# Kernel tuning notes

Measured on AMD Instinct MI355X. Metric: run time of the kernel, lower is better.

The kernel has to match this reference:

```python
import jax, jax.numpy as jnp
import numpy as np

DIM = 2048
DIM_SEQ = 2048
DIM_OUT = DIM // 2
LN_EPS = 1e-5


def setup_inputs() -> dict:
    key = jax.random.key(0)
    k1, k2 = jax.random.split(key)
    x = jax.random.normal(k1, (8, DIM_SEQ, DIM), dtype=jnp.float32)
    init_eps = 0.001 / DIM_SEQ
    # Conv1d(dim_seq, dim_seq, 1) weight -> [seq, seq] seq-mixing matrix
    proj_w = jax.random.uniform(k2, (DIM_SEQ, DIM_SEQ), minval=-init_eps, maxval=init_eps, dtype=jnp.float32)
    proj_b = jnp.ones((DIM_SEQ,), dtype=jnp.float32)
    ln_scale = jnp.ones((DIM_OUT,), dtype=jnp.float32)
    ln_bias = jnp.zeros((DIM_OUT,), dtype=jnp.float32)
    return {"x": x, "proj_w": proj_w, "proj_b": proj_b, "ln_scale": ln_scale, "ln_bias": ln_bias}


def reference(x, proj_w, proj_b, ln_scale, ln_bias):
    # chunk into residual and gate halves along feature dim
    res, gate = jnp.split(x, 2, axis=-1)  # each [b, s, d/2]
    # LayerNorm over last dim of gate
    mu = jnp.mean(gate, axis=-1, keepdims=True)
    var = jnp.mean(jnp.square(gate - mu), axis=-1, keepdims=True)
    gate = (gate - mu) * jax.lax.rsqrt(var + LN_EPS) * ln_scale + ln_bias
    # Conv1d kernel=1 over seq axis == seq-mixing matmul: [s,t] x [b,t,d] -> [b,s,d]
    gate = jnp.einsum('st,btd->bsd', proj_w, gate) + proj_b[None, :, None]
    # act = Identity; gated residual multiply
    return gate * res
```

## Files before the change

### kernel.cpp

```cpp
#include <hip/hip_runtime.h>

typedef __attribute__((ext_vector_type(8))) short short8;
typedef __attribute__((ext_vector_type(4))) float floatx4;

__device__ __forceinline__ unsigned short f2bf(float f) {
    unsigned int u = __builtin_bit_cast(unsigned int, f);
    u += 0x7fffu + ((u >> 16) & 1u);
    return (unsigned short)(u >> 16);
}

__device__ __forceinline__ void async16(unsigned short* lds, const unsigned short* g) {
    __builtin_amdgcn_global_load_lds(
        (__attribute__((address_space(1))) void*)(g),
        (__attribute__((address_space(3))) void*)(lds),
        16, 0, 0);
}

#define DIM      2048
#define DSEQ     2048
#define DOUT     1024
#define NBATCH   8
#define NKB      (DSEQ / 32)

__global__ __launch_bounds__(256) void cast_w_kernel(const float* __restrict__ w,
                                                     unsigned short* __restrict__ o) {
    int i = (blockIdx.x * 256 + threadIdx.x) * 4;
    int s = i >> 11;
    int t = i & 2047;
    float4 v = *(const float4*)(w + i);
    unsigned int lo = (unsigned int)f2bf(v.x) | ((unsigned int)f2bf(v.y) << 16);
    unsigned int hi = (unsigned int)f2bf(v.z) | ((unsigned int)f2bf(v.w) << 16);
    unsigned short* dst = o + (((size_t)(t >> 5)) * DSEQ + s) * 32 + (t & 31);
    *(uint2*)dst = make_uint2(lo, hi);
}

__global__ __launch_bounds__(256) void ln_t_kernel(const float* __restrict__ X,
                                                   const float* __restrict__ lns,
                                                   const float* __restrict__ lnb,
                                                   unsigned short* __restrict__ Gt) {
    const int tid  = threadIdx.x;
    const int wave = tid >> 6;
    const int lane = tid & 63;
    const int t0   = blockIdx.x * 32;
    const int b    = blockIdx.y;

    __shared__ unsigned short lt[32][1028];

    #pragma unroll
    for (int i = 0; i < 8; ++i) {
        const int r = wave * 8 + i;
        const float* xr = X + ((size_t)(b * DSEQ + t0 + r)) * DIM + DOUT;
        float4 v[4];
        float s = 0.f, ss = 0.f;
        #pragma unroll
        for (int c = 0; c < 4; ++c) {
            v[c] = *(const float4*)(xr + c * 256 + lane * 4);
            s  += v[c].x + v[c].y + v[c].z + v[c].w;
            ss += v[c].x * v[c].x + v[c].y * v[c].y + v[c].z * v[c].z + v[c].w * v[c].w;
        }
        #pragma unroll
        for (int off = 32; off > 0; off >>= 1) {
            s  += __shfl_xor(s,  off, 64);
            ss += __shfl_xor(ss, off, 64);
        }
        const float mu  = s * (1.f / 1024.f);
        const float var = ss * (1.f / 1024.f) - mu * mu;
        const float inv = rsqrtf(var + 1e-5f);
        #pragma unroll
        for (int c = 0; c < 4; ++c) {
            const int d = c * 256 + lane * 4;
            float4 sc = *(const float4*)(lns + d);
            float4 bi = *(const float4*)(lnb + d);
            float y0 = (v[c].x - mu) * inv * sc.x + bi.x;
            float y1 = (v[c].y - mu) * inv * sc.y + bi.y;
            float y2 = (v[c].z - mu) * inv * sc.z + bi.z;
            float y3 = (v[c].w - mu) * inv * sc.w + bi.w;
            unsigned int lo = (unsigned int)f2bf(y0) | ((unsigned int)f2bf(y1) << 16);
            unsigned int hi = (unsigned int)f2bf(y2) | ((unsigned int)f2bf(y3) << 16);
            *(uint2*)&lt[r][d] = make_uint2(lo, hi);
        }
    }
    __syncthreads();

    #pragma unroll
    for (int it = 0; it < 4; ++it) {
        const int d = it * 256 + tid;
        unsigned int u[16];
        #pragma unroll
        for (int j = 0; j < 16; ++j)
            u[j] = (unsigned int)lt[2 * j][d] | ((unsigned int)lt[2 * j + 1][d] << 16);
        uint4* dst = (uint4*)(Gt + (((size_t)b * NKB + (t0 >> 5)) * DOUT + d) * 32);
        dst[0] = make_uint4(u[0],  u[1],  u[2],  u[3]);
        dst[1] = make_uint4(u[4],  u[5],  u[6],  u[7]);
        dst[2] = make_uint4(u[8],  u[9],  u[10], u[11]);
        dst[3] = make_uint4(u[12], u[13], u[14], u[15]);
    }
}

#define BM 128
#define BN 128
#define BK 64

__global__ __launch_bounds__(256) void gemm_sgu(const unsigned short* __restrict__ Wt,
                                                const unsigned short* __restrict__ Gt,
                                                const float* __restrict__ X,
                                                const float* __restrict__ Pb,
                                                float* __restrict__ Out) {
    const int tid = threadIdx.x;
    const int s0  = blockIdx.x * BM;
    const int d0  = blockIdx.y * BN;
    const int b   = blockIdx.z;

    __shared__ unsigned short As[2 * BM * 32];
    __shared__ unsigned short Bs[2 * BN * 32];

    const int wave = tid >> 6;
    const int lane = tid & 63;
    const int wr   = wave >> 1;
    const int wc   = wave & 1;
    const int ln15 = lane & 15;
    const int q    = lane >> 4;

    floatx4 acc[4][4] = {};

    for (int k0 = 0; k0 < DSEQ; k0 += BK) {
        const int kb = k0 >> 5;
        const unsigned short* aG = Wt + ((size_t)kb * DSEQ + s0) * 32;
        const unsigned short* bG = Gt + (((size_t)b * NKB + kb) * DOUT + d0) * 32;

        __syncthreads();
        #pragma unroll
        for (int j = 0; j < 2; ++j) {
            const int ch = tid + j * 256;
            async16(&As[(size_t)ch * 8],        aG + (size_t)ch * 8);
            async16(&As[4096 + (size_t)ch * 8], aG + (size_t)DSEQ * 32 + (size_t)ch * 8);
            async16(&Bs[(size_t)ch * 8],        bG + (size_t)ch * 8);
            async16(&Bs[4096 + (size_t)ch * 8], bG + (size_t)DOUT * 32 + (size_t)ch * 8);
        }
        __syncthreads();

        #pragma unroll
        for (int u = 0; u < 2; ++u) {
            short8 af[4], bf[4];
            #pragma unroll
            for (int i = 0; i < 4; ++i)
                af[i] = *(const short8*)&As[(u * BM + wr * 64 + i * 16 + ln15) * 32 + q * 8];
            #pragma unroll
            for (int i = 0; i < 4; ++i)
                bf[i] = *(const short8*)&Bs[(u * BN + wc * 64 + i * 16 + ln15) * 32 + q * 8];
            #pragma unroll
            for (int i = 0; i < 4; ++i)
                #pragma unroll
                for (int j = 0; j < 4; ++j)
                    acc[i][j] = __builtin_amdgcn_mfma_f32_16x16x32_bf16(af[i], bf[j], acc[i][j], 0, 0, 0);
        }
    }

    #pragma unroll
    for (int i = 0; i < 4; ++i) {
        const int srow = s0 + wr * 64 + i * 16 + q * 4;
        #pragma unroll
        for (int j = 0; j < 4; ++j) {
            const int d = d0 + wc * 64 + j * 16 + ln15;
            #pragma unroll
            for (int r = 0; r < 4; ++r) {
                const int s = srow + r;
                const float g = acc[i][j][r] + Pb[s];
                const size_t xi = ((size_t)(b * DSEQ + s)) * DIM + d;
                const size_t oi = ((size_t)(b * DSEQ + s)) * DOUT + d;
                Out[oi] = g * X[xi];
            }
        }
    }
}

extern "C" void kernel_launch(void* const* d_in, const int* in_sizes, int n_in,
                              void* d_out, int out_size, void* d_ws, size_t ws_size,
                              hipStream_t stream) {
    const float* x    = (const float*)d_in[0];
    const float* pw   = (const float*)d_in[1];
    const float* pb   = (const float*)d_in[2];
    const float* lns  = (const float*)d_in[3];
    const float* lnb  = (const float*)d_in[4];
    float* out        = (float*)d_out;

    unsigned short* Wt = (unsigned short*)d_ws;
    unsigned short* Gt = (unsigned short*)((char*)d_ws + (size_t)DSEQ * DSEQ * 2);

    cast_w_kernel<<<dim3((DSEQ * DSEQ) / 1024), dim3(256), 0, stream>>>(pw, Wt);
    ln_t_kernel<<<dim3(DSEQ / 32, NBATCH), dim3(256), 0, stream>>>(x, lns, lnb, Gt);
    gemm_sgu<<<dim3(DSEQ / BM, DOUT / BN, NBATCH), dim3(256), 0, stream>>>(Wt, Gt, x, pb, out);
}
```

Before: 313.6 us.

## Swizzle GEMM LDS tiles with XOR layout and hoist LN params

The GEMM's shared-memory tiles become 64-element-wide rows. The 16-byte chunks within each row are XOR-swizzled by row index, and the async global-to-LDS load offsets and fragment read offsets are precomputed to match. This targets LDS bank conflicts on the short8 fragment reads. The LayerNorm kernel now loads the scale and bias once per thread instead of once per row, with its row loop no longer unrolled. The epilogue reads the projection bias as a float4 instead of a scalar per row.

```diff
diff --git a/kernel.cpp b/kernel.cpp
--- a/kernel.cpp
+++ b/kernel.cpp
@@ -46,7 +46,14 @@
 
     __shared__ unsigned short lt[32][1028];
 
-    #pragma unroll
+    float4 sc[4], bi[4];
+    #pragma unroll
+    for (int c = 0; c < 4; ++c) {
+        sc[c] = *(const float4*)(lns + c * 256 + lane * 4);
+        bi[c] = *(const float4*)(lnb + c * 256 + lane * 4);
+    }
+
+    #pragma unroll 1
     for (int i = 0; i < 8; ++i) {
         const int r = wave * 8 + i;
         const float* xr = X + ((size_t)(b * DSEQ + t0 + r)) * DIM + DOUT;
@@ -69,12 +76,10 @@
         #pragma unroll
         for (int c = 0; c < 4; ++c) {
             const int d = c * 256 + lane * 4;
-            float4 sc = *(const float4*)(lns + d);
-            float4 bi = *(const float4*)(lnb + d);
-            float y0 = (v[c].x - mu) * inv * sc.x + bi.x;
-            float y1 = (v[c].y - mu) * inv * sc.y + bi.y;
-            float y2 = (v[c].z - mu) * inv * sc.z + bi.z;
-            float y3 = (v[c].w - mu) * inv * sc.w + bi.w;
+            float y0 = (v[c].x - mu) * inv * sc[c].x + bi[c].x;
+            float y1 = (v[c].y - mu) * inv * sc[c].y + bi[c].y;
+            float y2 = (v[c].z - mu) * inv * sc[c].z + bi[c].z;
+            float y3 = (v[c].w - mu) * inv * sc[c].w + bi[c].w;
             unsigned int lo = (unsigned int)f2bf(y0) | ((unsigned int)f2bf(y1) << 16);
             unsigned int hi = (unsigned int)f2bf(y2) | ((unsigned int)f2bf(y3) << 16);
             *(uint2*)&lt[r][d] = make_uint2(lo, hi);
@@ -111,8 +116,8 @@
     const int d0  = blockIdx.y * BN;
     const int b   = blockIdx.z;
 
-    __shared__ unsigned short As[2 * BM * 32];
-    __shared__ unsigned short Bs[2 * BN * 32];
+    __shared__ unsigned short As[BM * 64];
+    __shared__ unsigned short Bs[BN * 64];
 
     const int wave = tid >> 6;
     const int lane = tid & 63;
@@ -121,21 +126,41 @@
     const int ln15 = lane & 15;
     const int q    = lane >> 4;
 
+    int ldsOff[4], srcA[4], srcB[4];
+    #pragma unroll
+    for (int j = 0; j < 4; ++j) {
+        const int c   = tid + j * 256;
+        const int r   = c >> 3;
+        const int kc  = (c & 7) ^ (r & 7);
+        const int u   = kc >> 2;
+        const int cc  = kc & 3;
+        ldsOff[j] = c * 8;
+        srcA[j]   = (u * DSEQ + s0 + r) * 32 + cc * 8;
+        srcB[j]   = (u * DOUT + d0 + r) * 32 + cc * 8;
+    }
+    int aOff[2][4], bOff[2][4];
+    #pragma unroll
+    for (int u = 0; u < 2; ++u)
+        #pragma unroll
+        for (int i = 0; i < 4; ++i) {
+            const int ra = wr * 64 + i * 16 + ln15;
+            const int rb = wc * 64 + i * 16 + ln15;
+            aOff[u][i] = ra * 64 + (((u * 4 + q) ^ (ra & 7)) * 8);
+            bOff[u][i] = rb * 64 + (((u * 4 + q) ^ (rb & 7)) * 8);
+        }
+
     floatx4 acc[4][4] = {};
 
-    for (int k0 = 0; k0 < DSEQ; k0 += BK) {
-        const int kb = k0 >> 5;
-        const unsigned short* aG = Wt + ((size_t)kb * DSEQ + s0) * 32;
-        const unsigned short* bG = Gt + (((size_t)b * NKB + kb) * DOUT + d0) * 32;
-
+    const unsigned short* gB = Gt + (size_t)b * NKB * DOUT * 32;
+
+    for (int kb = 0; kb < NKB; kb += 2) {
+        const unsigned short* aBase = Wt + (size_t)kb * DSEQ * 32;
+        const unsigned short* bBase = gB + (size_t)kb * DOUT * 32;
         __syncthreads();
         #pragma unroll
-        for (int j = 0; j < 2; ++j) {
-            const int ch = tid + j * 256;
-            async16(&As[(size_t)ch * 8],        aG + (size_t)ch * 8);
-            async16(&As[4096 + (size_t)ch * 8], aG + (size_t)DSEQ * 32 + (size_t)ch * 8);
-            async16(&Bs[(size_t)ch * 8],        bG + (size_t)ch * 8);
-            async16(&Bs[4096 + (size_t)ch * 8], bG + (size_t)DOUT * 32 + (size_t)ch * 8);
+        for (int j = 0; j < 4; ++j) {
+            async16(&As[ldsOff[j]], aBase + srcA[j]);
+            async16(&Bs[ldsOff[j]], bBase + srcB[j]);
         }
         __syncthreads();
 
@@ -143,11 +168,9 @@
         for (int u = 0; u < 2; ++u) {
             short8 af[4], bf[4];
             #pragma unroll
-            for (int i = 0; i < 4; ++i)
-                af[i] = *(const short8*)&As[(u * BM + wr * 64 + i * 16 + ln15) * 32 + q * 8];
-            #pragma unroll
-            for (int i = 0; i < 4; ++i)
-                bf[i] = *(const short8*)&Bs[(u * BN + wc * 64 + i * 16 + ln15) * 32 + q * 8];
+            for (int i = 0; i < 4; ++i) af[i] = *(const short8*)&As[aOff[u][i]];
+            #pragma unroll
+            for (int i = 0; i < 4; ++i) bf[i] = *(const short8*)&Bs[bOff[u][i]];
             #pragma unroll
             for (int i = 0; i < 4; ++i)
                 #pragma unroll
@@ -159,13 +182,14 @@
     #pragma unroll
     for (int i = 0; i < 4; ++i) {
         const int srow = s0 + wr * 64 + i * 16 + q * 4;
+        const float4 pb4 = *(const float4*)(Pb + srow);
         #pragma unroll
         for (int j = 0; j < 4; ++j) {
             const int d = d0 + wc * 64 + j * 16 + ln15;
             #pragma unroll
             for (int r = 0; r < 4; ++r) {
                 const int s = srow + r;
-                const float g = acc[i][j][r] + Pb[s];
+                const float g = acc[i][j][r] + ((const float*)&pb4)[r];
                 const size_t xi = ((size_t)(b * DSEQ + s)) * DIM + d;
                 const size_t oi = ((size_t)(b * DSEQ + s)) * DOUT + d;
                 Out[oi] = g * X[xi];
```

Result: no change. 311.6 us (-0.6%).
